# Kernel tuning notes

Measured on AMD Instinct MI355X. Metric: run time of the kernel, lower is better.

The kernel has to match this reference:

```python
import jax, jax.numpy as jnp
import numpy as np

D = 3       # in_out_dim
HID = 64    # hidden_dim
WIDTH = 64  # planar flow width
BATCH = 500000
BLOCK = D * WIDTH  # 192


def setup_inputs() -> dict:
    key = jax.random.key(0)
    ks = jax.random.split(key, 9)
    s1 = 1.0                      # fan_in=1
    s2 = 1.0 / np.sqrt(HID)
    return {
        "t": jax.random.uniform(ks[0], (1,), dtype=jnp.float32),
        "z": jax.random.normal(ks[1], (BATCH, D), dtype=jnp.float32),
        "logp_z": jnp.zeros((BATCH, 1), dtype=jnp.float32),
        "fc1_w": jax.random.normal(ks[2], (HID, 1), dtype=jnp.float32) * s1,
        "fc1_b": jax.random.normal(ks[3], (HID,), dtype=jnp.float32) * s1,
        "fc2_w": jax.random.normal(ks[4], (HID, HID), dtype=jnp.float32) * s2,
        "fc2_b": jax.random.normal(ks[5], (HID,), dtype=jnp.float32) * s2,
        "fc3_w": jax.random.normal(ks[6], (3 * BLOCK + WIDTH, HID), dtype=jnp.float32) * s2,
        "fc3_b": jax.random.normal(ks[7], (3 * BLOCK + WIDTH,), dtype=jnp.float32) * s2,
    }


def _hypernet(t, fc1_w, fc1_b, fc2_w, fc2_b, fc3_w, fc3_b):
    p = t.reshape(1, 1)
    p = jnp.tanh(p @ fc1_w.T + fc1_b)
    p = jnp.tanh(p @ fc2_w.T + fc2_b)
    p = (p @ fc3_w.T + fc3_b).reshape(-1)          # [3*BLOCK + WIDTH]
    W = p[:BLOCK].reshape(WIDTH, D)                # w_k vectors
    U = p[BLOCK:2 * BLOCK].reshape(WIDTH, D)
    G = p[2 * BLOCK:3 * BLOCK].reshape(WIDTH, D)
    U = U * jax.nn.sigmoid(G)                      # gated u_k vectors
    B = p[3 * BLOCK:]                              # [WIDTH] biases
    return W, B, U


def reference(t, z, logp_z, fc1_w, fc1_b, fc2_w, fc2_b, fc3_w, fc3_b):
    W, B, U = _hypernet(t, fc1_w, fc1_b, fc2_w, fc2_b, fc3_w, fc3_b)
    # h_k(z) = tanh(z . w_k + b_k)  -> [BATCH, WIDTH]
    h = jnp.tanh(z @ W.T + B)
    # dz/dt = mean_k h_k * u_k -> [BATCH, D]
    dz_dt = (h @ U) / WIDTH
    # trace of d(dz_dt)/dz, closed form: mean_k (1 - h_k^2) * (w_k . u_k)
    wu = jnp.sum(W * U, axis=1)                    # [WIDTH]
    trace = ((1.0 - h * h) @ wu) / WIDTH           # [BATCH]
    dlogp_z_dt = -trace[:, None]                   # [BATCH, 1]
    return dz_dt, dlogp_z_dt
```

## Files before the change

kernel.cpp:

```cpp
#include <hip/hip_runtime.h>
#include <math.h>

#define D      3
#define HID    64
#define WIDTH  64
#define BATCH  500000
#define BLOCKP (D * WIDTH)
#define NPAR   (3 * BLOCKP + WIDTH)
#define NCHUNK (BATCH / 4)

typedef float f2 __attribute__((ext_vector_type(2)));

__device__ __forceinline__ f2 sp(float s) { f2 r; r.x = s; r.y = s; return r; }
__device__ __forceinline__ f2 vfma(f2 a, f2 b, f2 c) {
    return __builtin_elementwise_fma(a, b, c);
}

__global__ __launch_bounds__(256) void cnf_kernel(
    const float* __restrict__ t,
    const float* __restrict__ z,
    const float* __restrict__ fc1_w, const float* __restrict__ fc1_b,
    const float* __restrict__ fc2_w, const float* __restrict__ fc2_b,
    const float* __restrict__ fc3_w, const float* __restrict__ fc3_b,
    float* __restrict__ out)
{
    __shared__ float p1[HID];
    __shared__ float p2[HID];
    __shared__ float p3[NPAR];
    __shared__ float4 pA[WIDTH];
    __shared__ float4 pB[WIDTH];

    const int tid = threadIdx.x;

    if (tid < HID) {
        p1[tid] = tanhf(t[0] * fc1_w[tid] + fc1_b[tid]);
    }
    __syncthreads();
    if (tid < HID) {
        const float* wrow = fc2_w + tid * HID;
        float a0 = 0.f, a1 = 0.f, a2 = 0.f, a3 = 0.f;
        #pragma unroll
        for (int k = 0; k < HID; k += 4) {
            a0 = fmaf(wrow[k + 0], p1[k + 0], a0);
            a1 = fmaf(wrow[k + 1], p1[k + 1], a1);
            a2 = fmaf(wrow[k + 2], p1[k + 2], a2);
            a3 = fmaf(wrow[k + 3], p1[k + 3], a3);
        }
        p2[tid] = tanhf(((a0 + a1) + (a2 + a3)) + fc2_b[tid]);
    }
    __syncthreads();
    for (int o = tid; o < NPAR; o += blockDim.x) {
        float acc = fc3_b[o];
        const float4* w4 = (const float4*)(fc3_w + o * HID);
        const float4* q4 = (const float4*)p2;
        #pragma unroll
        for (int k = 0; k < HID / 4; ++k) {
            float4 w = w4[k];
            float4 q = q4[k];
            acc += w.x * q.x + w.y * q.y + w.z * q.z + w.w * q.w;
        }
        p3[o] = acc;
    }
    __syncthreads();
    if (tid < WIDTH) {
        float W0 = p3[3 * tid + 0], W1 = p3[3 * tid + 1], W2 = p3[3 * tid + 2];
        float U0 = p3[BLOCKP + 3 * tid + 0], U1 = p3[BLOCKP + 3 * tid + 1], U2 = p3[BLOCKP + 3 * tid + 2];
        float G0 = p3[2 * BLOCKP + 3 * tid + 0], G1 = p3[2 * BLOCKP + 3 * tid + 1], G2 = p3[2 * BLOCKP + 3 * tid + 2];
        float B  = p3[3 * BLOCKP + tid];
        U0 *= 1.0f / (1.0f + expf(-G0));
        U1 *= 1.0f / (1.0f + expf(-G1));
        U2 *= 1.0f / (1.0f + expf(-G2));
        float wu = W0 * U0 + W1 * U1 + W2 * U2;
        const float c = 2.8853900817779268f;
        const float s = 1.0f / (float)WIDTH;
        pA[tid] = make_float4(W0 * c, W1 * c, W2 * c, B * c);
        pB[tid] = make_float4(U0 * s, U1 * s, U2 * s, -wu * s);
    }
    __syncthreads();

    const int gtid = blockIdx.x * blockDim.x + tid;
    if (gtid >= NCHUNK) return;

    const float4* z4 = (const float4*)z + (size_t)gtid * 3;
    float4 za = z4[0], zb = z4[1], zc = z4[2];
    f2 z0p[2], z1p[2], z2p[2];
    z0p[0] = (f2){za.x, za.w}; z0p[1] = (f2){zb.z, zc.y};
    z1p[0] = (f2){za.y, zb.x}; z1p[1] = (f2){zb.w, zc.z};
    z2p[0] = (f2){za.z, zb.y}; z2p[1] = (f2){zc.x, zc.w};

    f2 dz0[2] = {sp(0.f), sp(0.f)};
    f2 dz1[2] = {sp(0.f), sp(0.f)};
    f2 dz2[2] = {sp(0.f), sp(0.f)};
    f2 tr[2]  = {sp(0.f), sp(0.f)};

    #pragma unroll 4
    for (int j = 0; j < WIDTH; ++j) {
        float4 a = pA[j];
        float4 b = pB[j];

        f2 xa = vfma(z0p[0], sp(a.x), vfma(z1p[0], sp(a.y), vfma(z2p[0], sp(a.z), sp(a.w))));
        f2 xb = vfma(z0p[1], sp(a.x), vfma(z1p[1], sp(a.y), vfma(z2p[1], sp(a.z), sp(a.w))));
        xa = __builtin_elementwise_min(xa, sp(30.0f));
        xb = __builtin_elementwise_min(xb, sp(30.0f));

        f2 da, db;
        da.x = __builtin_amdgcn_exp2f(xa.x);
        da.y = __builtin_amdgcn_exp2f(xa.y);
        db.x = __builtin_amdgcn_exp2f(xb.x);
        db.y = __builtin_amdgcn_exp2f(xb.y);
        da = da + sp(1.0f);
        db = db + sp(1.0f);

        f2 q = da * db;
        float R = __builtin_amdgcn_rcpf(q.x * q.y);
        f2 rq; rq.x = R * q.y; rq.y = R * q.x;
        f2 inva = rq * db;
        f2 invb = rq * da;

        f2 ha = vfma(sp(-2.0f), inva, sp(1.0f));
        f2 hb = vfma(sp(-2.0f), invb, sp(1.0f));
        f2 ga = vfma(-ha, ha, sp(1.0f));
        f2 gb = vfma(-hb, hb, sp(1.0f));

        dz0[0] = vfma(ha, sp(b.x), dz0[0]);  dz0[1] = vfma(hb, sp(b.x), dz0[1]);
        dz1[0] = vfma(ha, sp(b.y), dz1[0]);  dz1[1] = vfma(hb, sp(b.y), dz1[1]);
        dz2[0] = vfma(ha, sp(b.z), dz2[0]);  dz2[1] = vfma(hb, sp(b.z), dz2[1]);
        tr[0]  = vfma(ga, sp(b.w), tr[0]);   tr[1]  = vfma(gb, sp(b.w), tr[1]);
    }

    float4* o4 = (float4*)out + (size_t)gtid * 3;
    o4[0] = make_float4(dz0[0].x, dz1[0].x, dz2[0].x, dz0[0].y);
    o4[1] = make_float4(dz1[0].y, dz2[0].y, dz0[1].x, dz1[1].x);
    o4[2] = make_float4(dz2[1].x, dz0[1].y, dz1[1].y, dz2[1].y);

    float4* l4 = (float4*)(out + 3 * BATCH);
    l4[gtid] = make_float4(tr[0].x, tr[0].y, tr[1].x, tr[1].y);
}

extern "C" void kernel_launch(void* const* d_in, const int* in_sizes, int n_in,
                              void* d_out, int out_size, void* d_ws, size_t ws_size,
                              hipStream_t stream) {
    const float* t     = (const float*)d_in[0];
    const float* z     = (const float*)d_in[1];
    const float* fc1_w = (const float*)d_in[3];
    const float* fc1_b = (const float*)d_in[4];
    const float* fc2_w = (const float*)d_in[5];
    const float* fc2_b = (const float*)d_in[6];
    const float* fc3_w = (const float*)d_in[7];
    const float* fc3_b = (const float*)d_in[8];
    float* out = (float*)d_out;

    const int threads = 256;
    const int blocks  = (NCHUNK + threads - 1) / threads;
    cnf_kernel<<<blocks, threads, 0, stream>>>(
        t, z, fc1_w, fc1_b, fc2_w, fc2_b, fc3_w, fc3_b, out);
}
```

Before: 95.08 us.

## Split hypernetwork into single-block kernel and halve per-thread batch work

The hypernetwork MLP, which every block used to recompute redundantly (including the 640x64 fc3 matvec), now runs once in a separate one-block kernel that writes the packed W/B and U/wu tables to the workspace. The main kernel only loads those 128 float4s into shared memory. Each thread now handles 2 samples instead of 4, doubling the grid for more parallelism and shorter tails. The cost is a second kernel launch with a serial dependency, and a shared reciprocal amortized over two samples instead of four.

```diff
diff --git a/kernel.cpp b/kernel.cpp
--- a/kernel.cpp
+++ b/kernel.cpp
@@ -7,7 +7,7 @@
 #define BATCH  500000
 #define BLOCKP (D * WIDTH)
 #define NPAR   (3 * BLOCKP + WIDTH)
-#define NCHUNK (BATCH / 4)
+#define NPAIR  (BATCH / 2)
 
 typedef float f2 __attribute__((ext_vector_type(2)));
 
@@ -16,19 +16,16 @@
     return __builtin_elementwise_fma(a, b, c);
 }
 
-__global__ __launch_bounds__(256) void cnf_kernel(
+__global__ __launch_bounds__(256) void hyper_kernel(
     const float* __restrict__ t,
-    const float* __restrict__ z,
     const float* __restrict__ fc1_w, const float* __restrict__ fc1_b,
     const float* __restrict__ fc2_w, const float* __restrict__ fc2_b,
     const float* __restrict__ fc3_w, const float* __restrict__ fc3_b,
-    float* __restrict__ out)
+    float4* __restrict__ par)
 {
     __shared__ float p1[HID];
     __shared__ float p2[HID];
     __shared__ float p3[NPAR];
-    __shared__ float4 pA[WIDTH];
-    __shared__ float4 pB[WIDTH];
 
     const int tid = threadIdx.x;
 
@@ -73,68 +70,68 @@
         float wu = W0 * U0 + W1 * U1 + W2 * U2;
         const float c = 2.8853900817779268f;
         const float s = 1.0f / (float)WIDTH;
-        pA[tid] = make_float4(W0 * c, W1 * c, W2 * c, B * c);
-        pB[tid] = make_float4(U0 * s, U1 * s, U2 * s, -wu * s);
+        par[tid]         = make_float4(W0 * c, W1 * c, W2 * c, B * c);
+        par[WIDTH + tid] = make_float4(U0 * s, U1 * s, U2 * s, -wu * s);
     }
+}
+
+__global__ __launch_bounds__(256) void cnf_main(
+    const float* __restrict__ z,
+    const float4* __restrict__ par,
+    float* __restrict__ out)
+{
+    __shared__ float4 stab[2 * WIDTH];
+
+    const int tid = threadIdx.x;
+    if (tid < 2 * WIDTH) stab[tid] = par[tid];
     __syncthreads();
 
-    const int gtid = blockIdx.x * blockDim.x + tid;
-    if (gtid >= NCHUNK) return;
+    const int gid = blockIdx.x * blockDim.x + tid;
+    if (gid >= NPAIR) return;
 
-    const float4* z4 = (const float4*)z + (size_t)gtid * 3;
-    float4 za = z4[0], zb = z4[1], zc = z4[2];
-    f2 z0p[2], z1p[2], z2p[2];
-    z0p[0] = (f2){za.x, za.w}; z0p[1] = (f2){zb.z, zc.y};
-    z1p[0] = (f2){za.y, zb.x}; z1p[1] = (f2){zb.w, zc.z};
-    z2p[0] = (f2){za.z, zb.y}; z2p[1] = (f2){zc.x, zc.w};
+    const f2* zp = (const f2*)z + (size_t)gid * 3;
+    f2 v0 = zp[0], v1 = zp[1], v2 = zp[2];
+    f2 z0 = {v0.x, v1.y};
+    f2 z1 = {v0.y, v2.x};
+    f2 z2 = {v1.x, v2.y};
 
-    f2 dz0[2] = {sp(0.f), sp(0.f)};
-    f2 dz1[2] = {sp(0.f), sp(0.f)};
-    f2 dz2[2] = {sp(0.f), sp(0.f)};
-    f2 tr[2]  = {sp(0.f), sp(0.f)};
+    f2 dz0 = sp(0.f), dz1 = sp(0.f), dz2 = sp(0.f), tr = sp(0.f);
 
-    #pragma unroll 4
+    const float4* sA = stab;
+    const float4* sB = stab + WIDTH;
+
+    #pragma unroll 8
     for (int j = 0; j < WIDTH; ++j) {
-        float4 a = pA[j];
-        float4 b = pB[j];
+        float4 a = sA[j];
+        float4 b = sB[j];
 
-        f2 xa = vfma(z0p[0], sp(a.x), vfma(z1p[0], sp(a.y), vfma(z2p[0], sp(a.z), sp(a.w))));
-        f2 xb = vfma(z0p[1], sp(a.x), vfma(z1p[1], sp(a.y), vfma(z2p[1], sp(a.z), sp(a.w))));
-        xa = __builtin_elementwise_min(xa, sp(30.0f));
-        xb = __builtin_elementwise_min(xb, sp(30.0f));
+        f2 x = vfma(z0, sp(a.x), vfma(z1, sp(a.y), vfma(z2, sp(a.z), sp(a.w))));
+        x = __builtin_elementwise_min(x, sp(30.0f));
 
-        f2 da, db;
-        da.x = __builtin_amdgcn_exp2f(xa.x);
-        da.y = __builtin_amdgcn_exp2f(xa.y);
-        db.x = __builtin_amdgcn_exp2f(xb.x);
-        db.y = __builtin_amdgcn_exp2f(xb.y);
-        da = da + sp(1.0f);
-        db = db + sp(1.0f);
+        f2 d;
+        d.x = __builtin_amdgcn_exp2f(x.x);
+        d.y = __builtin_amdgcn_exp2f(x.y);
+        d = d + sp(1.0f);
 
-        f2 q = da * db;
-        float R = __builtin_amdgcn_rcpf(q.x * q.y);
-        f2 rq; rq.x = R * q.y; rq.y = R * q.x;
-        f2 inva = rq * db;
-        f2 invb = rq * da;
+        float R = __builtin_amdgcn_rcpf(d.x * d.y);
+        f2 inv; inv.x = R * d.y; inv.y = R * d.x;
 
-        f2 ha = vfma(sp(-2.0f), inva, sp(1.0f));
-        f2 hb = vfma(sp(-2.0f), invb, sp(1.0f));
-        f2 ga = vfma(-ha, ha, sp(1.0f));
-        f2 gb = vfma(-hb, hb, sp(1.0f));
+        f2 h  = vfma(sp(-2.0f), inv, sp(1.0f));
+        f2 g1 = vfma(-h, h, sp(1.0f));
 
-        dz0[0] = vfma(ha, sp(b.x), dz0[0]);  dz0[1] = vfma(hb, sp(b.x), dz0[1]);
-        dz1[0] = vfma(ha, sp(b.y), dz1[0]);  dz1[1] = vfma(hb, sp(b.y), dz1[1]);
-        dz2[0] = vfma(ha, sp(b.z), dz2[0]);  dz2[1] = vfma(hb, sp(b.z), dz2[1]);
-        tr[0]  = vfma(ga, sp(b.w), tr[0]);   tr[1]  = vfma(gb, sp(b.w), tr[1]);
+        dz0 = vfma(h,  sp(b.x), dz0);
+        dz1 = vfma(h,  sp(b.y), dz1);
+        dz2 = vfma(h,  sp(b.z), dz2);
+        tr  = vfma(g1, sp(b.w), tr);
     }
 
-    float4* o4 = (float4*)out + (size_t)gtid * 3;
-    o4[0] = make_float4(dz0[0].x, dz1[0].x, dz2[0].x, dz0[0].y);
-    o4[1] = make_float4(dz1[0].y, dz2[0].y, dz0[1].x, dz1[1].x);
-    o4[2] = make_float4(dz2[1].x, dz0[1].y, dz1[1].y, dz2[1].y);
+    f2* o = (f2*)out + (size_t)gid * 3;
+    f2 w0 = {dz0.x, dz1.x};
+    f2 w1 = {dz2.x, dz0.y};
+    f2 w2 = {dz1.y, dz2.y};
+    o[0] = w0; o[1] = w1; o[2] = w2;
 
-    float4* l4 = (float4*)(out + 3 * BATCH);
-    l4[gtid] = make_float4(tr[0].x, tr[0].y, tr[1].x, tr[1].y);
+    ((f2*)(out + 3 * BATCH))[gid] = tr;
 }
 
 extern "C" void kernel_launch(void* const* d_in, const int* in_sizes, int n_in,
@@ -150,8 +147,12 @@
     const float* fc3_b = (const float*)d_in[8];
     float* out = (float*)d_out;
 
+    float4* par = (float4*)d_ws;
+
+    hyper_kernel<<<1, 256, 0, stream>>>(
+        t, fc1_w, fc1_b, fc2_w, fc2_b, fc3_w, fc3_b, par);
+
     const int threads = 256;
-    const int blocks  = (NCHUNK + threads - 1) / threads;
-    cnf_kernel<<<blocks, threads, 0, stream>>>(
-        t, z, fc1_w, fc1_b, fc2_w, fc2_b, fc3_w, fc3_b, out);
+    const int blocks  = (NPAIR + threads - 1) / threads;
+    cnf_main<<<blocks, threads, 0, stream>>>(z, par, out);
 }
```

After: 94.13 us. Within noise of the previous version (-1.0%).
